# Kernel optimization log

Hardware: AMD Instinct MI355X
Metric: run time of the kernel (lower is better)

The kernel has to match this reference:

```python
import math
import jax, jax.numpy as jnp
import numpy as np

EMBED_SIZE = 1024
NUM_HEADS = 16
HEAD_DIM = EMBED_SIZE // NUM_HEADS
N, L = 8, 1024
MASK_FILL = -1e3  # value used by masked_fill in the original (NOT -inf)
SCALE = 1.0 / math.sqrt(EMBED_SIZE)  # original divides by embed_size**0.5, not head_dim


def setup_inputs() -> dict:
    key = jax.random.key(0)
    ks = jax.random.split(key, 7)
    values = jax.random.normal(ks[0], (N, L, EMBED_SIZE), dtype=jnp.float32)
    keys_t = jax.random.normal(ks[1], (N, L, EMBED_SIZE), dtype=jnp.float32)
    queries = jax.random.normal(ks[2], (N, L, EMBED_SIZE), dtype=jnp.float32)
    attn_mask = jax.random.randint(ks[3], (1, 1, L, L), 0, 2, dtype=jnp.int32)
    scr_key_padding_mask = jax.random.randint(ks[4], (N, 1, 1, L), 0, 2, dtype=jnp.int32)
    # fc_out: nn.Linear(embed_size, embed_size) with bias
    fc_w = jax.random.normal(ks[5], (EMBED_SIZE, EMBED_SIZE), dtype=jnp.float32) * (1.0 / math.sqrt(EMBED_SIZE))
    fc_b = jax.random.normal(ks[6], (EMBED_SIZE,), dtype=jnp.float32) * 0.01
    return {"values": values, "keys": keys_t, "queries": queries,
            "fc_w": fc_w, "fc_b": fc_b,
            "attn_mask": attn_mask, "scr_key_padding_mask": scr_key_padding_mask}


def reference(values, keys, queries, fc_w, fc_b, attn_mask, scr_key_padding_mask):
    n, q_len, e = queries.shape
    k_len = keys.shape[1]
    h, d = NUM_HEADS, HEAD_DIM
    # NOTE: the original defines per-head Linear projections but never applies them
    v = values.reshape(n, k_len, h, d)
    k = keys.reshape(n, k_len, h, d)
    q = queries.reshape(n, q_len, h, d)
    energy = jnp.einsum('nqhd,nkhd->nhqk', q, k)  # [n, h, q, k]
    am = attn_mask[:, :, :k_len, :k_len]
    energy = jnp.where(am == 0, MASK_FILL, energy)
    energy = jnp.where(scr_key_padding_mask == 0, MASK_FILL, energy)
    attention = jax.nn.softmax(energy * SCALE, axis=3)
    out = jnp.einsum('nhql,nlhd->nqhd', attention, v).reshape(n, q_len, h * d)
    return out @ fc_w.T + fc_b
```

## Files before the change

kernel.cpp:

```cpp
#include <hip/hip_runtime.h>

#define L_SEQ 1024
#define EMB 1024
#define NH 16
#define HD 64

typedef _Float16 half8 __attribute__((ext_vector_type(8)));
typedef _Float16 half4v __attribute__((ext_vector_type(4)));
typedef float f32x4 __attribute__((ext_vector_type(4)));
typedef float fvec4 __attribute__((ext_vector_type(4)));
typedef unsigned int u32;
typedef unsigned long long u64;

constexpr float C2 = 0.045084220027780106f;
constexpr float F2 = -45.08422002778011f;

constexpr int FP = 40;
constexpr int PP = 72;

__device__ __forceinline__ void async16(const void* g, void* l) {
    __builtin_amdgcn_global_load_lds((const __attribute__((address_space(1))) u32*)g,
                                     (__attribute__((address_space(3))) u32*)l, 16, 0, 0);
}

__global__ void pack_mask_kernel(const int* __restrict__ am, u32* __restrict__ bits) {
    const int i = blockIdx.x * 256 + threadIdx.x;
    const int lane = threadIdx.x & 63;
    u64 b = __ballot(am[i] != 0);
    if (lane == 0)       bits[i >> 5] = (u32)b;
    else if (lane == 32) bits[i >> 5] = (u32)(b >> 32);
}

__global__ void convert_w_kernel(const float* __restrict__ w, _Float16* __restrict__ o) {
    size_t i = ((size_t)blockIdx.x * blockDim.x + threadIdx.x) * 4;
    fvec4 v = *(const fvec4*)(w + i);
    half4v h;
#pragma unroll
    for (int j = 0; j < 4; ++j) h[j] = (_Float16)v[j];
    *(half4v*)(o + i) = h;
}

__global__ __launch_bounds__(256) void cvt_kv_kernel(
    const float* __restrict__ keys, const float* __restrict__ values,
    _Float16* __restrict__ K16, _Float16* __restrict__ Vt16)
{
    __shared__ __align__(16) _Float16 Vt[64 * PP];
    const int tid = threadIdx.x;
    const int kt = blockIdx.x, h = blockIdx.y, n = blockIdx.z;
    const int kbase = kt * 64;
    const int r = tid >> 2, c0 = (tid & 3) * 16;
    const int nh = n * NH + h;

    {
        const float* src = keys + ((size_t)(n * L_SEQ + kbase + r)) * EMB + h * HD + c0;
        fvec4 a0 = *(const fvec4*)(src),     a1 = *(const fvec4*)(src + 4);
        fvec4 a2 = *(const fvec4*)(src + 8), a3 = *(const fvec4*)(src + 12);
        half8 o0, o1;
#pragma unroll
        for (int j = 0; j < 4; ++j) {
            o0[j] = (_Float16)a0[j]; o0[j + 4] = (_Float16)a1[j];
            o1[j] = (_Float16)a2[j]; o1[j + 4] = (_Float16)a3[j];
        }
        _Float16* dst = K16 + ((size_t)nh * L_SEQ + kbase + r) * HD + c0;
        *(half8*)dst = o0; *(half8*)(dst + 8) = o1;
    }
    {
        const float* src = values + ((size_t)(n * L_SEQ + kbase + r)) * EMB + h * HD + c0;
        fvec4 vv[4];
        vv[0] = *(const fvec4*)(src);     vv[1] = *(const fvec4*)(src + 4);
        vv[2] = *(const fvec4*)(src + 8); vv[3] = *(const fvec4*)(src + 12);
#pragma unroll
        for (int i = 0; i < 16; ++i)
            Vt[(c0 + i) * PP + r] = (_Float16)vv[i >> 2][i & 3];
    }
    __syncthreads();
    {
        const int d = tid >> 2, k0 = (tid & 3) * 16;
        half8 v0 = *(const half8*)(&Vt[d * PP + k0]);
        half8 v1 = *(const half8*)(&Vt[d * PP + k0 + 8]);
        _Float16* dst = Vt16 + ((size_t)nh * HD + d) * L_SEQ + kbase + k0;
        *(half8*)dst = v0; *(half8*)(dst + 8) = v1;
    }
}

__global__ __launch_bounds__(256, 4) void attn_kernel(
    const _Float16* __restrict__ K16, const _Float16* __restrict__ Vt16,
    const float* __restrict__ queries, const u32* __restrict__ mbits,
    const int* __restrict__ pad_mask, _Float16* __restrict__ out_f16)
{
    __shared__ __align__(16) _Float16 K_lds[64 * 64];
    __shared__ __align__(16) _Float16 V_lds[64 * 64];
    __shared__ __align__(16) _Float16 P_lds[128 * PP];

    const int tid = threadIdx.x;
    const int lane = tid & 63;
    const int wave = tid >> 6;
    const int l16 = lane & 15;
    const int quad = lane >> 4;
    const int bid = blockIdx.x;
    const int nh = bid & 127, qt = bid >> 7;
    const int n = nh >> 4, h = nh & 15;
    const int qbase = qt * 128;
    const int xr = l16 & 7;

    half8 qf[2][2];
#pragma unroll
    for (int s = 0; s < 2; ++s) {
        const int qrow = qbase + wave * 32 + s * 16 + l16;
        const float* qp = queries + ((size_t)(n * L_SEQ + qrow)) * EMB + h * HD;
#pragma unroll
        for (int t = 0; t < 2; ++t) {
            fvec4 a = *(const fvec4*)(qp + t * 32 + quad * 8);
            fvec4 b = *(const fvec4*)(qp + t * 32 + quad * 8 + 4);
#pragma unroll
            for (int j = 0; j < 4; ++j) { qf[s][t][j] = (_Float16)a[j]; qf[s][t][j + 4] = (_Float16)b[j]; }
        }
    }

    f32x4 Ov[2][4];
#pragma unroll
    for (int s = 0; s < 2; ++s)
#pragma unroll
        for (int dt = 0; dt < 4; ++dt) Ov[s][dt] = (f32x4){0.f, 0.f, 0.f, 0.f};
    float lsum[2] = {0.f, 0.f};

    const _Float16* Kt_base = K16 + (size_t)nh * L_SEQ * HD;
    const _Float16* Vt_base = Vt16 + (size_t)nh * HD * L_SEQ;
    const int gch = (lane & 7) ^ ((lane >> 3) & 7);

    for (int kt = 0; kt < L_SEQ / 64; ++kt) {
        const int kbase = kt * 64;
        u32 w0[2], w1[2];
#pragma unroll
        for (int s = 0; s < 2; ++s) {
            const int qrow = qbase + wave * 32 + s * 16 + l16;
            w0[s] = mbits[qrow * 32 + kt * 2];
            w1[s] = mbits[qrow * 32 + kt * 2 + 1];
        }
        const u64 bal = __ballot(pad_mask[(size_t)n * L_SEQ + kbase + lane] != 0);
        const u32 plo = (u32)bal, phi = (u32)(bal >> 32);

        __syncthreads();
#pragma unroll
        for (int s2 = 0; s2 < 2; ++s2) {
            const int row = wave * 16 + s2 * 8 + (lane >> 3);
            async16(Kt_base + (size_t)(kbase + row) * HD + gch * 8, &K_lds[(wave * 16 + s2 * 8) * 64]);
            async16(Vt_base + (size_t)row * L_SEQ + kbase + gch * 8, &V_lds[(wave * 16 + s2 * 8) * 64]);
        }
        __syncthreads();

        f32x4 S[2][4];
#pragma unroll
        for (int s = 0; s < 2; ++s)
#pragma unroll
            for (int tj = 0; tj < 4; ++tj) S[s][tj] = (f32x4){0.f, 0.f, 0.f, 0.f};
#pragma unroll
        for (int tj = 0; tj < 4; ++tj) {
            const int krow = tj * 16 + l16;
            const _Float16* kr = &K_lds[krow * 64];
            const int c0 = (quad ^ xr) * 8;
            half8 k0 = *(const half8*)(kr + c0);
            half8 k1 = *(const half8*)(kr + (c0 ^ 32));
            S[0][tj] = __builtin_amdgcn_mfma_f32_16x16x32_f16(k0, qf[0][0], S[0][tj], 0, 0, 0);
            S[0][tj] = __builtin_amdgcn_mfma_f32_16x16x32_f16(k1, qf[0][1], S[0][tj], 0, 0, 0);
            S[1][tj] = __builtin_amdgcn_mfma_f32_16x16x32_f16(k0, qf[1][0], S[1][tj], 0, 0, 0);
            S[1][tj] = __builtin_amdgcn_mfma_f32_16x16x32_f16(k1, qf[1][1], S[1][tj], 0, 0, 0);
        }

#pragma unroll
        for (int s = 0; s < 2; ++s) {
            const u32 pw0 = w0[s] & plo, pw1 = w1[s] & phi;
#pragma unroll
            for (int tj = 0; tj < 4; ++tj) {
                const u32 m4 = ((tj & 2) ? pw1 : pw0) >> ((tj & 1) * 16 + quad * 4);
                float p[4];
#pragma unroll
                for (int reg = 0; reg < 4; ++reg) {
                    const float e = ((m4 >> reg) & 1u) ? S[s][tj][reg] * C2 : F2;
                    p[reg] = __builtin_amdgcn_exp2f(e);
                }
                lsum[s] += (p[0] + p[1]) + (p[2] + p[3]);
                half4v hp = {(_Float16)p[0], (_Float16)p[1], (_Float16)p[2], (_Float16)p[3]};
                *(half4v*)(&P_lds[(wave * 32 + s * 16 + l16) * PP + tj * 16 + quad * 4]) = hp;
            }
        }

        half8 pf0[2], pf1[2];
#pragma unroll
        for (int t = 0; t < 2; ++t) {
            pf0[t] = *(const half8*)(&P_lds[(wave * 32 + l16) * PP + t * 32 + quad * 8]);
            pf1[t] = *(const half8*)(&P_lds[(wave * 32 + 16 + l16) * PP + t * 32 + quad * 8]);
        }
#pragma unroll
        for (int t = 0; t < 2; ++t) {
            const int c0 = ((t * 4 + quad) ^ xr) * 8;
#pragma unroll
            for (int dt = 0; dt < 4; ++dt) {
                half8 vf = *(const half8*)(&V_lds[(dt * 16 + l16) * 64 + c0]);
                Ov[0][dt] = __builtin_amdgcn_mfma_f32_16x16x32_f16(pf0[t], vf, Ov[0][dt], 0, 0, 0);
                Ov[1][dt] = __builtin_amdgcn_mfma_f32_16x16x32_f16(pf1[t], vf, Ov[1][dt], 0, 0, 0);
            }
        }
    }

#pragma unroll
    for (int s = 0; s < 2; ++s) {
        lsum[s] += __shfl_xor(lsum[s], 16);
        lsum[s] += __shfl_xor(lsum[s], 32);
    }
#pragma unroll
    for (int s = 0; s < 2; ++s)
#pragma unroll
        for (int reg = 0; reg < 4; ++reg) {
            const float linv = 1.0f / __shfl(lsum[s], quad * 4 + reg);
            const int qrow = qbase + wave * 32 + s * 16 + quad * 4 + reg;
            _Float16* op = out_f16 + ((size_t)(n * L_SEQ + qrow)) * EMB + h * HD;
#pragma unroll
            for (int dt = 0; dt < 4; ++dt)
                op[dt * 16 + l16] = (_Float16)(Ov[s][dt][reg] * linv);
        }
}

__global__ __launch_bounds__(256) void fc_kernel(
    const _Float16* __restrict__ A, const _Float16* __restrict__ W,
    const float* __restrict__ bias, float* __restrict__ C)
{
    __shared__ __align__(16) _Float16 As[128 * FP];
    __shared__ __align__(16) _Float16 Ws[128 * FP];

    const int tid = threadIdx.x;
    const int lane = tid & 63;
    const int wv = tid >> 6;
    const int l16 = lane & 15;
    const int quad = lane >> 4;
    const int wm = (wv >> 1) * 64, wn = (wv & 1) * 64;
    const int Mb = blockIdx.x * 128, Nb = blockIdx.y * 128;

    f32x4 acc[4][4];
#pragma unroll
    for (int i = 0; i < 4; ++i)
#pragma unroll
        for (int j = 0; j < 4; ++j) acc[i][j] = (f32x4){0.f, 0.f, 0.f, 0.f};

    for (int k0 = 0; k0 < EMB; k0 += 32) {
        __syncthreads();
#pragma unroll
        for (int s = 0; s < 2; ++s) {
            const int id = tid + s * 256;
            const int row = id >> 2, ch = (id & 3) * 8;
            *(half8*)(&As[row * FP + ch]) = *(const half8*)(A + (size_t)(Mb + row) * EMB + k0 + ch);
            *(half8*)(&Ws[row * FP + ch]) = *(const half8*)(W + (size_t)(Nb + row) * EMB + k0 + ch);
        }
        __syncthreads();

        half8 af[4], bf[4];
#pragma unroll
        for (int i = 0; i < 4; ++i) {
            af[i] = *(const half8*)(&As[(wm + i * 16 + l16) * FP + quad * 8]);
            bf[i] = *(const half8*)(&Ws[(wn + i * 16 + l16) * FP + quad * 8]);
        }
#pragma unroll
        for (int i = 0; i < 4; ++i)
#pragma unroll
            for (int j = 0; j < 4; ++j)
                acc[i][j] = __builtin_amdgcn_mfma_f32_16x16x32_f16(af[i], bf[j], acc[i][j], 0, 0, 0);
    }

#pragma unroll
    for (int i = 0; i < 4; ++i) {
        const int m = Mb + wm + i * 16 + quad * 4;
#pragma unroll
        for (int j = 0; j < 4; ++j) {
            const int jc = Nb + wn + j * 16 + l16;
            const float b = bias[jc];
#pragma unroll
            for (int reg = 0; reg < 4; ++reg)
                C[(size_t)(m + reg) * EMB + jc] = acc[i][j][reg] + b;
        }
    }
}

extern "C" void kernel_launch(void* const* d_in, const int* in_sizes, int n_in,
                              void* d_out, int out_size, void* d_ws, size_t ws_size,
                              hipStream_t stream) {
    const float* values  = (const float*)d_in[0];
    const float* keys    = (const float*)d_in[1];
    const float* queries = (const float*)d_in[2];
    const float* fc_w    = (const float*)d_in[3];
    const float* fc_b    = (const float*)d_in[4];
    const int*   amask   = (const int*)d_in[5];
    const int*   pmask   = (const int*)d_in[6];
    float* out = (float*)d_out;

    char* w = (char*)d_ws;
    _Float16* attn_out = (_Float16*)w;
    _Float16* w_f16    = (_Float16*)(w + (size_t)16 * 1024 * 1024);
    u32*      mbits    = (u32*)(w + (size_t)18 * 1024 * 1024);
    _Float16* K16      = (_Float16*)(w + (size_t)19 * 1024 * 1024);
    _Float16* Vt16     = (_Float16*)(w + (size_t)35 * 1024 * 1024);

    pack_mask_kernel<<<4096, 256, 0, stream>>>(amask, mbits);
    convert_w_kernel<<<1024, 256, 0, stream>>>(fc_w, w_f16);
    cvt_kv_kernel<<<dim3(16, 16, 8), 256, 0, stream>>>(keys, values, K16, Vt16);
    attn_kernel<<<1024, 256, 0, stream>>>(K16, Vt16, queries, mbits, pmask, attn_out);
    fc_kernel<<<dim3(64, 8), 256, 0, stream>>>(attn_out, w_f16, fc_b, out);
}
```

Baseline: 240.7 us.

## Double-buffer attention K/V tiles, precombine masks, fold scale into Q, async FC loads

The attention kernel now double-buffers K/V tiles in LDS. It prefetches the next tile with async global-to-LDS loads while computing the current one, which removes one barrier per iteration. The attention and padding masks are ANDed into a per-batch bitmask by a new small kernel, and the softmax scale is folded into Q at load time. The FC kernel moves to a K-step of 64 with swizzled async LDS loads. Doubling LDS and lowering launch bounds to 3 reduces occupancy, and there is an extra kernel launch.

```diff
diff --git a/kernel.cpp b/kernel.cpp
--- a/kernel.cpp
+++ b/kernel.cpp
@@ -15,7 +15,6 @@
 constexpr float C2 = 0.045084220027780106f;
 constexpr float F2 = -45.08422002778011f;
 
-constexpr int FP = 40;
 constexpr int PP = 72;
 
 __device__ __forceinline__ void async16(const void* g, void* l) {
@@ -31,6 +30,18 @@
     else if (lane == 32) bits[i >> 5] = (u32)(b >> 32);
 }
 
+__global__ void combine_mask_kernel(const u32* __restrict__ abits,
+                                    const u32* __restrict__ pbits,
+                                    u32* __restrict__ cmb) {
+    const int tid = threadIdx.x;
+    const int w = tid & 31, qq = tid >> 5;
+    const int q = blockIdx.x * 8 + qq;
+    const u32 a = abits[q * 32 + w];
+#pragma unroll
+    for (int n = 0; n < 8; ++n)
+        cmb[((size_t)(n * L_SEQ) + q) * 32 + w] = a & pbits[n * 32 + w];
+}
+
 __global__ void convert_w_kernel(const float* __restrict__ w, _Float16* __restrict__ o) {
     size_t i = ((size_t)blockIdx.x * blockDim.x + threadIdx.x) * 4;
     fvec4 v = *(const fvec4*)(w + i);
@@ -42,7 +53,8 @@
 
 __global__ __launch_bounds__(256) void cvt_kv_kernel(
     const float* __restrict__ keys, const float* __restrict__ values,
-    _Float16* __restrict__ K16, _Float16* __restrict__ Vt16)
+    const int* __restrict__ pad_mask,
+    _Float16* __restrict__ K16, _Float16* __restrict__ Vt16, u32* __restrict__ pbits)
 {
     __shared__ __align__(16) _Float16 Vt[64 * PP];
     const int tid = threadIdx.x;
@@ -73,6 +85,11 @@
         for (int i = 0; i < 16; ++i)
             Vt[(c0 + i) * PP + r] = (_Float16)vv[i >> 2][i & 3];
     }
+    if (blockIdx.y == 0 && tid < 64) {
+        u64 b = __ballot(pad_mask[(size_t)n * L_SEQ + kbase + tid] != 0);
+        if (tid == 0)       pbits[n * 32 + kt * 2]     = (u32)b;
+        else if (tid == 32) pbits[n * 32 + kt * 2 + 1] = (u32)(b >> 32);
+    }
     __syncthreads();
     {
         const int d = tid >> 2, k0 = (tid & 3) * 16;
@@ -83,13 +100,13 @@
     }
 }
 
-__global__ __launch_bounds__(256, 4) void attn_kernel(
+__global__ __launch_bounds__(256, 3) void attn_kernel(
     const _Float16* __restrict__ K16, const _Float16* __restrict__ Vt16,
-    const float* __restrict__ queries, const u32* __restrict__ mbits,
-    const int* __restrict__ pad_mask, _Float16* __restrict__ out_f16)
+    const float* __restrict__ queries, const u32* __restrict__ cmb,
+    _Float16* __restrict__ out_f16)
 {
-    __shared__ __align__(16) _Float16 K_lds[64 * 64];
-    __shared__ __align__(16) _Float16 V_lds[64 * 64];
+    __shared__ __align__(16) _Float16 K_lds[2][64 * 64];
+    __shared__ __align__(16) _Float16 V_lds[2][64 * 64];
     __shared__ __align__(16) _Float16 P_lds[128 * PP];
 
     const int tid = threadIdx.x;
@@ -113,7 +130,10 @@
             fvec4 a = *(const fvec4*)(qp + t * 32 + quad * 8);
             fvec4 b = *(const fvec4*)(qp + t * 32 + quad * 8 + 4);
 #pragma unroll
-            for (int j = 0; j < 4; ++j) { qf[s][t][j] = (_Float16)a[j]; qf[s][t][j + 4] = (_Float16)b[j]; }
+            for (int j = 0; j < 4; ++j) {
+                qf[s][t][j]     = (_Float16)(a[j] * C2);
+                qf[s][t][j + 4] = (_Float16)(b[j] * C2);
+            }
         }
     }
 
@@ -127,27 +147,34 @@
     const _Float16* Kt_base = K16 + (size_t)nh * L_SEQ * HD;
     const _Float16* Vt_base = Vt16 + (size_t)nh * HD * L_SEQ;
     const int gch = (lane & 7) ^ ((lane >> 3) & 7);
+    const int drow = (lane >> 3);
+    const u32* mrow0 = cmb + ((size_t)(n * L_SEQ) + qbase + wave * 32 + l16) * 32;
+    const u32* mrow1 = mrow0 + 16 * 32;
+
+#pragma unroll
+    for (int s2 = 0; s2 < 2; ++s2) {
+        const int row = wave * 16 + s2 * 8 + drow;
+        async16(Kt_base + (size_t)row * HD + gch * 8, &K_lds[0][(wave * 16 + s2 * 8) * 64]);
+        async16(Vt_base + (size_t)row * L_SEQ + gch * 8, &V_lds[0][(wave * 16 + s2 * 8) * 64]);
+    }
 
     for (int kt = 0; kt < L_SEQ / 64; ++kt) {
-        const int kbase = kt * 64;
-        u32 w0[2], w1[2];
-#pragma unroll
-        for (int s = 0; s < 2; ++s) {
-            const int qrow = qbase + wave * 32 + s * 16 + l16;
-            w0[s] = mbits[qrow * 32 + kt * 2];
-            w1[s] = mbits[qrow * 32 + kt * 2 + 1];
-        }
-        const u64 bal = __ballot(pad_mask[(size_t)n * L_SEQ + kbase + lane] != 0);
-        const u32 plo = (u32)bal, phi = (u32)(bal >> 32);
-
+        const int cb = kt & 1;
         __syncthreads();
-#pragma unroll
-        for (int s2 = 0; s2 < 2; ++s2) {
-            const int row = wave * 16 + s2 * 8 + (lane >> 3);
-            async16(Kt_base + (size_t)(kbase + row) * HD + gch * 8, &K_lds[(wave * 16 + s2 * 8) * 64]);
-            async16(Vt_base + (size_t)row * L_SEQ + kbase + gch * 8, &V_lds[(wave * 16 + s2 * 8) * 64]);
-        }
-        __syncthreads();
+
+        if (kt < 15) {
+            const int kb2 = (kt + 1) * 64;
+#pragma unroll
+            for (int s2 = 0; s2 < 2; ++s2) {
+                const int row = wave * 16 + s2 * 8 + drow;
+                async16(Kt_base + (size_t)(kb2 + row) * HD + gch * 8,
+                        &K_lds[cb ^ 1][(wave * 16 + s2 * 8) * 64]);
+                async16(Vt_base + (size_t)row * L_SEQ + kb2 + gch * 8,
+                        &V_lds[cb ^ 1][(wave * 16 + s2 * 8) * 64]);
+            }
+        }
+        const u32 w0a = mrow0[kt * 2], w1a = mrow0[kt * 2 + 1];
+        const u32 w0b = mrow1[kt * 2], w1b = mrow1[kt * 2 + 1];
 
         f32x4 S[2][4];
 #pragma unroll
@@ -156,8 +183,7 @@
             for (int tj = 0; tj < 4; ++tj) S[s][tj] = (f32x4){0.f, 0.f, 0.f, 0.f};
 #pragma unroll
         for (int tj = 0; tj < 4; ++tj) {
-            const int krow = tj * 16 + l16;
-            const _Float16* kr = &K_lds[krow * 64];
+            const _Float16* kr = &K_lds[cb][(tj * 16 + l16) * 64];
             const int c0 = (quad ^ xr) * 8;
             half8 k0 = *(const half8*)(kr + c0);
             half8 k1 = *(const half8*)(kr + (c0 ^ 32));
@@ -169,14 +195,14 @@
 
 #pragma unroll
         for (int s = 0; s < 2; ++s) {
-            const u32 pw0 = w0[s] & plo, pw1 = w1[s] & phi;
+            const u32 pw0 = s ? w0b : w0a, pw1 = s ? w1b : w1a;
 #pragma unroll
             for (int tj = 0; tj < 4; ++tj) {
                 const u32 m4 = ((tj & 2) ? pw1 : pw0) >> ((tj & 1) * 16 + quad * 4);
                 float p[4];
 #pragma unroll
                 for (int reg = 0; reg < 4; ++reg) {
-                    const float e = ((m4 >> reg) & 1u) ? S[s][tj][reg] * C2 : F2;
+                    const float e = ((m4 >> reg) & 1u) ? S[s][tj][reg] : F2;
                     p[reg] = __builtin_amdgcn_exp2f(e);
                 }
                 lsum[s] += (p[0] + p[1]) + (p[2] + p[3]);
@@ -196,7 +222,7 @@
             const int c0 = ((t * 4 + quad) ^ xr) * 8;
 #pragma unroll
             for (int dt = 0; dt < 4; ++dt) {
-                half8 vf = *(const half8*)(&V_lds[(dt * 16 + l16) * 64 + c0]);
+                half8 vf = *(const half8*)(&V_lds[cb][(dt * 16 + l16) * 64 + c0]);
                 Ov[0][dt] = __builtin_amdgcn_mfma_f32_16x16x32_f16(pf0[t], vf, Ov[0][dt], 0, 0, 0);
                 Ov[1][dt] = __builtin_amdgcn_mfma_f32_16x16x32_f16(pf1[t], vf, Ov[1][dt], 0, 0, 0);
             }
@@ -221,12 +247,12 @@
         }
 }
 
-__global__ __launch_bounds__(256) void fc_kernel(
+__global__ __launch_bounds__(256, 3) void fc_kernel(
     const _Float16* __restrict__ A, const _Float16* __restrict__ W,
     const float* __restrict__ bias, float* __restrict__ C)
 {
-    __shared__ __align__(16) _Float16 As[128 * FP];
-    __shared__ __align__(16) _Float16 Ws[128 * FP];
+    __shared__ __align__(16) _Float16 As[128 * 64];
+    __shared__ __align__(16) _Float16 Ws[128 * 64];
 
     const int tid = threadIdx.x;
     const int lane = tid & 63;
@@ -235,6 +261,9 @@
     const int quad = lane >> 4;
     const int wm = (wv >> 1) * 64, wn = (wv & 1) * 64;
     const int Mb = blockIdx.x * 128, Nb = blockIdx.y * 128;
+    const int gch = (lane & 7) ^ ((lane >> 3) & 7);
+    const int drow = lane >> 3;
+    const int xr = l16 & 7;
 
     f32x4 acc[4][4];
 #pragma unroll
@@ -242,28 +271,31 @@
 #pragma unroll
         for (int j = 0; j < 4; ++j) acc[i][j] = (f32x4){0.f, 0.f, 0.f, 0.f};
 
-    for (int k0 = 0; k0 < EMB; k0 += 32) {
+    for (int k0 = 0; k0 < EMB; k0 += 64) {
         __syncthreads();
 #pragma unroll
-        for (int s = 0; s < 2; ++s) {
-            const int id = tid + s * 256;
-            const int row = id >> 2, ch = (id & 3) * 8;
-            *(half8*)(&As[row * FP + ch]) = *(const half8*)(A + (size_t)(Mb + row) * EMB + k0 + ch);
-            *(half8*)(&Ws[row * FP + ch]) = *(const half8*)(W + (size_t)(Nb + row) * EMB + k0 + ch);
+        for (int s = 0; s < 4; ++s) {
+            const int row = wv * 32 + s * 8 + drow;
+            async16(A + (size_t)(Mb + row) * EMB + k0 + gch * 8, &As[(wv * 32 + s * 8) * 64]);
+            async16(W + (size_t)(Nb + row) * EMB + k0 + gch * 8, &Ws[(wv * 32 + s * 8) * 64]);
         }
         __syncthreads();
 
-        half8 af[4], bf[4];
-#pragma unroll
-        for (int i = 0; i < 4; ++i) {
-            af[i] = *(const half8*)(&As[(wm + i * 16 + l16) * FP + quad * 8]);
-            bf[i] = *(const half8*)(&Ws[(wn + i * 16 + l16) * FP + quad * 8]);
-        }
-#pragma unroll
-        for (int i = 0; i < 4; ++i)
-#pragma unroll
-            for (int j = 0; j < 4; ++j)
-                acc[i][j] = __builtin_amdgcn_mfma_f32_16x16x32_f16(af[i], bf[j], acc[i][j], 0, 0, 0);
+#pragma unroll
+        for (int t = 0; t < 2; ++t) {
+            half8 af[4], bf[4];
+            const int c0 = ((t * 4 + quad) ^ xr) * 8;
+#pragma unroll
+            for (int i = 0; i < 4; ++i) {
+                af[i] = *(const half8*)(&As[(wm + i * 16 + l16) * 64 + c0]);
+                bf[i] = *(const half8*)(&Ws[(wn + i * 16 + l16) * 64 + c0]);
+            }
+#pragma unroll
+            for (int i = 0; i < 4; ++i)
+#pragma unroll
+                for (int j = 0; j < 4; ++j)
+                    acc[i][j] = __builtin_amdgcn_mfma_f32_16x16x32_f16(af[i], bf[j], acc[i][j], 0, 0, 0);
+        }
     }
 
 #pragma unroll
@@ -295,13 +327,16 @@
     char* w = (char*)d_ws;
     _Float16* attn_out = (_Float16*)w;
     _Float16* w_f16    = (_Float16*)(w + (size_t)16 * 1024 * 1024);
-    u32*      mbits    = (u32*)(w + (size_t)18 * 1024 * 1024);
-    _Float16* K16      = (_Float16*)(w + (size_t)19 * 1024 * 1024);
-    _Float16* Vt16     = (_Float16*)(w + (size_t)35 * 1024 * 1024);
-
-    pack_mask_kernel<<<4096, 256, 0, stream>>>(amask, mbits);
+    u32*      abits    = (u32*)(w + (size_t)18 * 1024 * 1024);
+    u32*      pbits    = (u32*)(w + (size_t)18 * 1024 * 1024 + 512 * 1024);
+    u32*      cmb      = (u32*)(w + (size_t)19 * 1024 * 1024);
+    _Float16* K16      = (_Float16*)(w + (size_t)20 * 1024 * 1024);
+    _Float16* Vt16     = (_Float16*)(w + (size_t)36 * 1024 * 1024);
+
+    pack_mask_kernel<<<4096, 256, 0, stream>>>(amask, abits);
     convert_w_kernel<<<1024, 256, 0, stream>>>(fc_w, w_f16);
-    cvt_kv_kernel<<<dim3(16, 16, 8), 256, 0, stream>>>(keys, values, K16, Vt16);
-    attn_kernel<<<1024, 256, 0, stream>>>(K16, Vt16, queries, mbits, pmask, attn_out);
+    cvt_kv_kernel<<<dim3(16, 16, 8), 256, 0, stream>>>(keys, values, pmask, K16, Vt16, pbits);
+    combine_mask_kernel<<<128, 256, 0, stream>>>(abits, pbits, cmb);
+    attn_kernel<<<1024, 256, 0, stream>>>(K16, Vt16, queries, cmb, attn_out);
     fc_kernel<<<dim3(64, 8), 256, 0, stream>>>(attn_out, w_f16, fc_b, out);
 }
```

New measurement: 242.6 us. About the same (+0.8%).
